# Kernel tuning notes

Hardware: AMD Instinct MI355X
Metric: run time of the kernel (lower is better)

Reference implementation:

```python
import jax, jax.numpy as jnp
import numpy as np

N = 100000   # total nodes in batched graph
E = 400000   # directed edges
F0 = 64      # Drug_Features
B = 512      # number of graphs
FINAL = 128  # Final_dim


def setup_inputs() -> dict:
    key = jax.random.key(0)
    ks = jax.random.split(key, 24)
    def w(k, shape, fan_in):
        return jax.random.normal(k, shape, dtype=jnp.float32) / np.sqrt(fan_in)
    inp = {
        "x": jax.random.normal(ks[0], (N, F0), dtype=jnp.float32),
        "edge_index": jax.random.randint(ks[1], (2, E), 0, N, dtype=jnp.int32),
        "batch": jnp.sort(jax.random.randint(ks[2], (N,), 0, B, dtype=jnp.int32)),
        "eps": jax.random.normal(ks[3], (N, 4 * F0), dtype=jnp.float32),
        # GCNConv weights: lin (in,out) no bias, separate bias added post-aggregation
        "W1": w(ks[4], (F0, 2 * F0), F0), "b1": jnp.zeros((2 * F0,), jnp.float32),
        "W2": w(ks[5], (2 * F0, 3 * F0), 2 * F0), "b2": jnp.zeros((3 * F0,), jnp.float32),
        "W3": w(ks[6], (3 * F0, 4 * F0), 3 * F0), "b3": jnp.zeros((4 * F0,), jnp.float32),
        "Wmu": w(ks[7], (4 * F0, 4 * F0), 4 * F0), "bmu": jnp.zeros((4 * F0,), jnp.float32),
        "Wlv": w(ks[8], (4 * F0, 4 * F0), 4 * F0), "blv": jnp.zeros((4 * F0,), jnp.float32),
        "fc1_w": w(ks[9], (4 * F0, 1024), 4 * F0), "fc1_b": jnp.zeros((1024,), jnp.float32),
        "fc2_w": w(ks[10], (1024, FINAL), 1024), "fc2_b": jnp.zeros((FINAL,), jnp.float32),
    }
    return inp


def reference(x, edge_index, batch, eps, W1, b1, W2, b2, W3, b3, Wmu, bmu, Wlv, blv,
              fc1_w, fc1_b, fc2_w, fc2_b):
    n = x.shape[0]
    row, col = edge_index[0], edge_index[1]
    loop = jnp.arange(n, dtype=row.dtype)
    row_f = jnp.concatenate([row, loop])  # with self-loops (PyG GCNConv default)
    col_f = jnp.concatenate([col, loop])
    deg = jax.ops.segment_sum(jnp.ones_like(col_f, dtype=x.dtype), col_f, num_segments=n)
    dinv = jnp.where(deg > 0, deg ** -0.5, 0.0)
    norm = (dinv[row_f] * dinv[col_f])[:, None]  # [E+N, 1]

    def gcn(h, W, b):
        m = h @ W                                   # transform first (out <= in here ok)
        agg = jax.ops.segment_sum(norm * m[row_f], col_f, num_segments=n)
        return agg + b

    h = jax.nn.relu(gcn(x, W1, b1))
    h = jax.nn.relu(gcn(h, W2, b2))
    h = jax.nn.relu(gcn(h, W3, b3))   # PMVO pre-pool features [N, 4F]
    mu = gcn(h, Wmu, bmu)
    logvar = gcn(h, Wlv, blv)
    std = jnp.exp(0.5 * logvar)
    amvo = mu + eps * std             # reparameterize
    x2 = jax.ops.segment_max(h, batch, num_segments=B)   # global max pool per graph
    pmvo = jax.nn.relu(x2 @ fc1_w + fc1_b) @ fc2_w + fc2_b  # dropout is identity (eval)
    return (amvo, mu, logvar, pmvo)
```

## Files before the change

### kernel.cpp

```cpp
#include <hip/hip_runtime.h>
#include <hip/hip_bf16.h>
#include <math.h>


#define THREADS 256

typedef short s8v __attribute__((ext_vector_type(8)));
typedef float f4v __attribute__((ext_vector_type(4)));

__device__ inline float bf_lo(unsigned int u) {
    union { unsigned int i; float f; } c; c.i = u << 16; return c.f;
}
__device__ inline float bf_hi(unsigned int u) {
    union { unsigned int i; float f; } c; c.i = u & 0xffff0000u; return c.f;
}
__device__ inline unsigned short f2bf(float f) {
    __hip_bfloat16 h = __float2bfloat16(f);
    return *reinterpret_cast<unsigned short*>(&h);
}
__device__ inline float bf2f(unsigned short u) {
    union { unsigned int i; float f; } c; c.i = ((unsigned int)u) << 16; return c.f;
}


__global__ void k_count(const int* __restrict__ col, int* __restrict__ counts, int E) {
    int e = blockIdx.x * blockDim.x + threadIdx.x;
    if (e < E) atomicAdd(&counts[col[e]], 1);
}

__global__ void k_dinv(const int* __restrict__ counts, float* __restrict__ dinv, int N) {
    int i = blockIdx.x * blockDim.x + threadIdx.x;
    if (i < N) dinv[i] = rsqrtf((float)(counts[i] + 1));
}

__global__ __launch_bounds__(1024) void k_scan(const int* __restrict__ counts,
                                               int* __restrict__ offsets, int N) {
    __shared__ int ssum[1024];
    int tid = threadIdx.x;
    int chunk = (N + 1023) / 1024;
    int begin = tid * chunk;
    int end = begin + chunk; if (end > N) end = N;
    int s = 0;
    for (int i = begin; i < end; ++i) s += counts[i] + 1;
    ssum[tid] = s;
    __syncthreads();
    for (int off = 1; off < 1024; off <<= 1) {
        int v = 0;
        if (tid >= off) v = ssum[tid - off];
        __syncthreads();
        if (tid >= off) ssum[tid] += v;
        __syncthreads();
    }
    int prefix = (tid == 0) ? 0 : ssum[tid - 1];
    for (int i = begin; i < end; ++i) {
        offsets[i] = prefix;
        prefix += counts[i] + 1;
    }
    if (end == N && begin < N) offsets[N] = prefix;
}

__global__ void k_init_cursor(const int* __restrict__ offsets, int* __restrict__ cursor, int N) {
    int i = blockIdx.x * blockDim.x + threadIdx.x;
    if (i < N) cursor[i] = offsets[i];
}

__global__ void k_scatter(const int* __restrict__ row, const int* __restrict__ col,
                          const float* __restrict__ dinv, int* __restrict__ cursor,
                          int* __restrict__ csr_row, float* __restrict__ csr_norm,
                          int E, int N) {
    int e = blockIdx.x * blockDim.x + threadIdx.x;
    if (e < E) {
        int r = row[e], c = col[e];
        int slot = atomicAdd(&cursor[c], 1);
        csr_row[slot] = r;
        csr_norm[slot] = dinv[r] * dinv[c];
    } else if (e < E + N) {
        int i = e - E;
        int slot = atomicAdd(&cursor[i], 1);
        csr_row[slot] = i;
        float d = dinv[i];
        csr_norm[slot] = d * d;
    }
}


__global__ void k_cast_bf16(const float* __restrict__ src, unsigned short* __restrict__ dst, int n) {
    int i = blockIdx.x * blockDim.x + threadIdx.x;
    if (i < n) dst[i] = f2bf(src[i]);
}

__global__ void k_prep_w(const float* __restrict__ W, unsigned short* __restrict__ WT,
                         int K, int Nc) {
    int id = blockIdx.x * blockDim.x + threadIdx.x;
    if (id < K * Nc) {
        int k = id / Nc, n = id % Nc;
        WT[(size_t)n * K + k] = f2bf(W[id]);
    }
}

__global__ void k_agg(const unsigned short* __restrict__ h,
                      const int* __restrict__ offsets,
                      const int* __restrict__ csr_row,
                      const float* __restrict__ csr_nrm,
                      unsigned short* __restrict__ g, int N, int F) {
    int node = blockIdx.x * blockDim.y + threadIdx.y;
    if (node >= N) return;
    int c8 = threadIdx.x * 8;
    int off0 = offsets[node], off1 = offsets[node + 1];
    float a0=0.f,a1=0.f,a2=0.f,a3=0.f,a4=0.f,a5=0.f,a6=0.f,a7=0.f;
    for (int sl = off0; sl < off1; ++sl) {
        int r = csr_row[sl];
        float w = csr_nrm[sl];
        uint4 v = *(const uint4*)(h + (size_t)r * F + c8);
        a0 += w * bf_lo(v.x); a1 += w * bf_hi(v.x);
        a2 += w * bf_lo(v.y); a3 += w * bf_hi(v.y);
        a4 += w * bf_lo(v.z); a5 += w * bf_hi(v.z);
        a6 += w * bf_lo(v.w); a7 += w * bf_hi(v.w);
    }
    uint4 o;
    o.x = (unsigned)f2bf(a0) | ((unsigned)f2bf(a1) << 16);
    o.y = (unsigned)f2bf(a2) | ((unsigned)f2bf(a3) << 16);
    o.z = (unsigned)f2bf(a4) | ((unsigned)f2bf(a5) << 16);
    o.w = (unsigned)f2bf(a6) | ((unsigned)f2bf(a7) << 16);
    *(uint4*)(g + (size_t)node * F + c8) = o;
}

#define GBM 128
#define GBN 64
#define GBK 64
#define LDP 72

__global__ __launch_bounds__(512) void k_gemm_mfma(
    const unsigned short* __restrict__ A,
    const unsigned short* __restrict__ WT,
    const float* __restrict__ bias,
    void* __restrict__ Cout, int M, int K, int Nc,
    int dorelu, int out_bf16) {
    __shared__ unsigned short sA[GBM * LDP];
    __shared__ unsigned short sB[GBN * LDP];
    const int tid = threadIdx.x;
    const int wave = tid >> 6;
    const int lane = tid & 63;
    const int bm = blockIdx.x * GBM;
    const int bn = blockIdx.y * GBN;

    f4v acc[4];
    #pragma unroll
    for (int j = 0; j < 4; ++j) acc[j] = (f4v){0.f, 0.f, 0.f, 0.f};

    const int lrow = tid >> 3;
    const int lk = (tid & 7) * 8;
    const int fr = lane & 15;
    const int fk = (lane >> 4) * 8;

    for (int k0 = 0; k0 < K; k0 += GBK) {
        #pragma unroll
        for (int p = 0; p < 2; ++p) {
            int r = lrow + p * 64;
            int gm = bm + r;
            uint4 v = make_uint4(0u, 0u, 0u, 0u);
            if (gm < M) v = *(const uint4*)(A + (size_t)gm * K + k0 + lk);
            *(uint4*)(&sA[r * LDP + lk]) = v;
        }
        {
            uint4 v = *(const uint4*)(WT + (size_t)(bn + lrow) * K + k0 + lk);
            *(uint4*)(&sB[lrow * LDP + lk]) = v;
        }
        __syncthreads();
        #pragma unroll
        for (int ks = 0; ks < 2; ++ks) {
            s8v a0 = *(const s8v*)(&sA[(wave * 16 + fr) * LDP + ks * 32 + fk]);
            #pragma unroll
            for (int nt = 0; nt < 4; ++nt) {
                s8v b = *(const s8v*)(&sB[(nt * 16 + fr) * LDP + ks * 32 + fk]);
                acc[nt] = __builtin_amdgcn_mfma_f32_16x16x32_bf16(a0, b, acc[nt], 0, 0, 0);
            }
        }
        __syncthreads();
    }

    const int col_l = lane & 15;
    const int row_q = (lane >> 4) * 4;
    #pragma unroll
    for (int nt = 0; nt < 4; ++nt) {
        #pragma unroll
        for (int i = 0; i < 4; ++i) {
            int row = bm + wave * 16 + row_q + i;
            int col = bn + nt * 16 + col_l;
            if (row < M) {
                float v = acc[nt][i] + bias[col];
                if (dorelu) v = fmaxf(v, 0.f);
                if (out_bf16)
                    ((unsigned short*)Cout)[(size_t)row * Nc + col] = f2bf(v);
                else
                    ((float*)Cout)[(size_t)row * Nc + col] = v;
            }
        }
    }
}

__global__ __launch_bounds__(512) void k_gemm_mfma_dual(
    const unsigned short* __restrict__ A,
    const unsigned short* __restrict__ WTm,
    const unsigned short* __restrict__ WTl,
    const float* __restrict__ bmu,
    const float* __restrict__ blv,
    const float* __restrict__ eps,
    float* __restrict__ mu,
    float* __restrict__ lv,
    float* __restrict__ amvo,
    int M, int K, int Nc) {
    __shared__ unsigned short sA[GBM * LDP];
    __shared__ unsigned short sBm[GBN * LDP];
    __shared__ unsigned short sBl[GBN * LDP];
    const int tid = threadIdx.x;
    const int wave = tid >> 6;
    const int lane = tid & 63;
    const int bm = blockIdx.x * GBM;
    const int bn = blockIdx.y * GBN;

    f4v accM[4], accL[4];
    #pragma unroll
    for (int j = 0; j < 4; ++j) {
        accM[j] = (f4v){0.f, 0.f, 0.f, 0.f};
        accL[j] = (f4v){0.f, 0.f, 0.f, 0.f};
    }

    const int lrow = tid >> 3;
    const int lk = (tid & 7) * 8;
    const int fr = lane & 15;
    const int fk = (lane >> 4) * 8;

    for (int k0 = 0; k0 < K; k0 += GBK) {
        #pragma unroll
        for (int p = 0; p < 2; ++p) {
            int r = lrow + p * 64;
            int gm = bm + r;
            uint4 v = make_uint4(0u, 0u, 0u, 0u);
            if (gm < M) v = *(const uint4*)(A + (size_t)gm * K + k0 + lk);
            *(uint4*)(&sA[r * LDP + lk]) = v;
        }
        {
            uint4 vm = *(const uint4*)(WTm + (size_t)(bn + lrow) * K + k0 + lk);
            uint4 vl = *(const uint4*)(WTl + (size_t)(bn + lrow) * K + k0 + lk);
            *(uint4*)(&sBm[lrow * LDP + lk]) = vm;
            *(uint4*)(&sBl[lrow * LDP + lk]) = vl;
        }
        __syncthreads();
        #pragma unroll
        for (int ks = 0; ks < 2; ++ks) {
            s8v a0 = *(const s8v*)(&sA[(wave * 16 + fr) * LDP + ks * 32 + fk]);
            #pragma unroll
            for (int nt = 0; nt < 4; ++nt) {
                s8v bm_ = *(const s8v*)(&sBm[(nt * 16 + fr) * LDP + ks * 32 + fk]);
                s8v bl_ = *(const s8v*)(&sBl[(nt * 16 + fr) * LDP + ks * 32 + fk]);
                accM[nt] = __builtin_amdgcn_mfma_f32_16x16x32_bf16(a0, bm_, accM[nt], 0, 0, 0);
                accL[nt] = __builtin_amdgcn_mfma_f32_16x16x32_bf16(a0, bl_, accL[nt], 0, 0, 0);
            }
        }
        __syncthreads();
    }

    const int col_l = lane & 15;
    const int row_q = (lane >> 4) * 4;
    #pragma unroll
    for (int nt = 0; nt < 4; ++nt) {
        int col = bn + nt * 16 + col_l;
        float bM = bmu[col];
        float bL = blv[col];
        #pragma unroll
        for (int i = 0; i < 4; ++i) {
            int row = bm + wave * 16 + row_q + i;
            if (row < M) {
                size_t idx = (size_t)row * Nc + col;
                float vm = accM[nt][i] + bM;
                float vl = accL[nt][i] + bL;
                mu[idx] = vm;
                lv[idx] = vl;
                amvo[idx] = vm + eps[idx] * expf(0.5f * vl);
            }
        }
    }
}

__global__ __launch_bounds__(256) void k_fc1(const float* __restrict__ x2,
                                             const float* __restrict__ W,
                                             const float* __restrict__ bias,
                                             float* __restrict__ hid,
                                             int K, int Nc) {
    const int m = blockIdx.x;
    const int t = threadIdx.x;
    __shared__ float sx[256];
    for (int k = t; k < K; k += 256) sx[k] = x2[(size_t)m * K + k];
    __syncthreads();
    const int nc4 = Nc >> 2;
    const float4* Wv = (const float4*)W;
    float4 acc = make_float4(0.f, 0.f, 0.f, 0.f);
    #pragma unroll 4
    for (int k = 0; k < K; ++k) {
        float a = sx[k];
        float4 w = Wv[(size_t)k * nc4 + t];
        acc.x += a * w.x; acc.y += a * w.y;
        acc.z += a * w.z; acc.w += a * w.w;
    }
    float4 b = ((const float4*)bias)[t];
    float4 r;
    r.x = fmaxf(acc.x + b.x, 0.f);
    r.y = fmaxf(acc.y + b.y, 0.f);
    r.z = fmaxf(acc.z + b.z, 0.f);
    r.w = fmaxf(acc.w + b.w, 0.f);
    ((float4*)hid)[(size_t)m * nc4 + t] = r;
}

__global__ __launch_bounds__(128) void k_fc2(const float* __restrict__ hid,
                                             const float* __restrict__ W,
                                             const float* __restrict__ bias,
                                             float* __restrict__ out,
                                             int K, int Nc) {
    const int m = blockIdx.x;
    const int c = threadIdx.x;
    __shared__ float sh[1024];
    for (int k = c; k < K; k += 128) sh[k] = hid[(size_t)m * K + k];
    __syncthreads();
    float a0 = 0.f, a1 = 0.f, a2 = 0.f, a3 = 0.f;
    for (int k = 0; k < K; k += 4) {
        a0 += sh[k    ] * W[(size_t)(k    ) * Nc + c];
        a1 += sh[k + 1] * W[(size_t)(k + 1) * Nc + c];
        a2 += sh[k + 2] * W[(size_t)(k + 2) * Nc + c];
        a3 += sh[k + 3] * W[(size_t)(k + 3) * Nc + c];
    }
    out[(size_t)m * Nc + c] = (a0 + a1) + (a2 + a3) + bias[c];
}


__global__ void k_gstart(const int* __restrict__ batch, int* __restrict__ gstart, int Nn, int B) {
    int b = blockIdx.x * blockDim.x + threadIdx.x;
    if (b > B) return;
    int lo = 0, hi = Nn;
    while (lo < hi) {
        int mid = (lo + hi) >> 1;
        if (batch[mid] < b) lo = mid + 1; else hi = mid;
    }
    gstart[b] = lo;
}

__global__ void k_pool_max(const unsigned short* __restrict__ h, const int* __restrict__ gstart,
                           float* __restrict__ x2, int F) {
    int b = blockIdx.x;
    int c = blockIdx.y * 64 + threadIdx.x;
    int s = gstart[b], e = gstart[b + 1];
    float mv = -INFINITY;
    for (int i = s + threadIdx.y; i < e; i += 4)
        mv = fmaxf(mv, bf2f(h[(size_t)i * F + c]));
    __shared__ float red[4][64];
    red[threadIdx.y][threadIdx.x] = mv;
    __syncthreads();
    if (threadIdx.y == 0) {
        mv = fmaxf(fmaxf(red[0][threadIdx.x], red[1][threadIdx.x]),
                   fmaxf(red[2][threadIdx.x], red[3][threadIdx.x]));
        x2[(size_t)b * F + c] = mv;
    }
}

static inline int ceil_div(int a, int b) { return (a + b - 1) / b; }

extern "C" void kernel_launch(void* const* d_in, const int* in_sizes, int n_in,
                              void* d_out, int out_size, void* d_ws, size_t ws_size,
                              hipStream_t stream) {
    const int F0 = 64;
    const int N = in_sizes[0] / F0;
    const int E = in_sizes[1] / 2;
    const int F4 = 4 * F0;
    const int B = (out_size - 3 * N * F4) / 128;
    const int M = E + N;

    const float* x     = (const float*)d_in[0];
    const int*   ei    = (const int*)d_in[1];
    const int*   batch = (const int*)d_in[2];
    const float* eps   = (const float*)d_in[3];
    const float* W1  = (const float*)d_in[4];  const float* b1  = (const float*)d_in[5];
    const float* W2  = (const float*)d_in[6];  const float* b2  = (const float*)d_in[7];
    const float* W3  = (const float*)d_in[8];  const float* b3  = (const float*)d_in[9];
    const float* Wmu = (const float*)d_in[10]; const float* bmu = (const float*)d_in[11];
    const float* Wlv = (const float*)d_in[12]; const float* blv = (const float*)d_in[13];
    const float* fc1w = (const float*)d_in[14]; const float* fc1b = (const float*)d_in[15];
    const float* fc2w = (const float*)d_in[16]; const float* fc2b = (const float*)d_in[17];

    const int* e_row = ei;
    const int* e_col = ei + E;

    float* out  = (float*)d_out;
    float* amvo = out;
    float* mu   = out + (size_t)N * F4;
    float* lv   = out + 2 * (size_t)N * F4;
    float* pmvo = out + 3 * (size_t)N * F4;

    char* w = (char*)d_ws;
    auto alloc = [&](size_t bytes) -> void* {
        void* p = (void*)w;
        w += (bytes + 255) & ~(size_t)255;
        return p;
    };
    float* dinv    = (float*)alloc((size_t)N * 4);
    int*   counts  = (int*)alloc((size_t)N * 4);
    int*   offsets = (int*)alloc((size_t)(N + 1) * 4);
    int*   csr_row = (int*)alloc((size_t)M * 4);
    float* csr_nrm = (float*)alloc((size_t)M * 4);
    int*   gstart  = (int*)alloc((size_t)(B + 1) * 4);
    unsigned short* xb  = (unsigned short*)alloc((size_t)N * F0 * 2);
    unsigned short* h1  = (unsigned short*)alloc((size_t)N * 128 * 2);
    unsigned short* h2  = (unsigned short*)alloc((size_t)N * 192 * 2);
    unsigned short* h3  = (unsigned short*)alloc((size_t)N * 256 * 2);
    unsigned short* g   = (unsigned short*)alloc((size_t)N * 256 * 2);
    unsigned short* wt1 = (unsigned short*)alloc((size_t)64 * 128 * 2);
    unsigned short* wt2 = (unsigned short*)alloc((size_t)128 * 192 * 2);
    unsigned short* wt3 = (unsigned short*)alloc((size_t)192 * 256 * 2);
    unsigned short* wtm = (unsigned short*)alloc((size_t)256 * 256 * 2);
    unsigned short* wtl = (unsigned short*)alloc((size_t)256 * 256 * 2);
    float* x2  = (float*)alloc((size_t)B * F4 * 4);
    float* hid = (float*)alloc((size_t)B * 1024 * 4);
    (void)ws_size; (void)n_in;

    hipMemsetAsync(counts, 0, (size_t)N * 4, stream);
    k_count<<<ceil_div(E, THREADS), THREADS, 0, stream>>>(e_col, counts, E);
    k_dinv<<<ceil_div(N, THREADS), THREADS, 0, stream>>>(counts, dinv, N);
    k_scan<<<1, 1024, 0, stream>>>(counts, offsets, N);
    k_init_cursor<<<ceil_div(N, THREADS), THREADS, 0, stream>>>(offsets, counts, N);
    k_scatter<<<ceil_div(E + N, THREADS), THREADS, 0, stream>>>(
        e_row, e_col, dinv, counts, csr_row, csr_nrm, E, N);

    k_cast_bf16<<<ceil_div(N * F0, THREADS), THREADS, 0, stream>>>(x, xb, N * F0);
    k_prep_w<<<ceil_div(64 * 128, THREADS), THREADS, 0, stream>>>(W1, wt1, 64, 128);
    k_prep_w<<<ceil_div(128 * 192, THREADS), THREADS, 0, stream>>>(W2, wt2, 128, 192);
    k_prep_w<<<ceil_div(192 * 256, THREADS), THREADS, 0, stream>>>(W3, wt3, 192, 256);
    k_prep_w<<<ceil_div(256 * 256, THREADS), THREADS, 0, stream>>>(Wmu, wtm, 256, 256);
    k_prep_w<<<ceil_div(256 * 256, THREADS), THREADS, 0, stream>>>(Wlv, wtl, 256, 256);

    {
        dim3 blk(8, 32);
        k_agg<<<ceil_div(N, 32), blk, 0, stream>>>(xb, offsets, csr_row, csr_nrm, g, N, 64);
        dim3 gg(ceil_div(N, GBM), 128 / GBN);
        k_gemm_mfma<<<gg, 512, 0, stream>>>(g, wt1, b1, h1, N, 64, 128, 1, 1);
    }
    {
        dim3 blk(16, 16);
        k_agg<<<ceil_div(N, 16), blk, 0, stream>>>(h1, offsets, csr_row, csr_nrm, g, N, 128);
        dim3 gg(ceil_div(N, GBM), 192 / GBN);
        k_gemm_mfma<<<gg, 512, 0, stream>>>(g, wt2, b2, h2, N, 128, 192, 1, 1);
    }
    {
        dim3 blk(24, 8);
        k_agg<<<ceil_div(N, 8), blk, 0, stream>>>(h2, offsets, csr_row, csr_nrm, g, N, 192);
        dim3 gg(ceil_div(N, GBM), 256 / GBN);
        k_gemm_mfma<<<gg, 512, 0, stream>>>(g, wt3, b3, h3, N, 192, 256, 1, 1);
    }
    {
        dim3 blk(32, 8);
        k_agg<<<ceil_div(N, 8), blk, 0, stream>>>(h3, offsets, csr_row, csr_nrm, g, N, 256);
        dim3 gg(ceil_div(N, GBM), 256 / GBN);
        k_gemm_mfma_dual<<<gg, 512, 0, stream>>>(g, wtm, wtl, bmu, blv, eps,
                                                 mu, lv, amvo, N, 256, 256);
    }

    k_gstart<<<ceil_div(B + 1, THREADS), THREADS, 0, stream>>>(batch, gstart, N, B);
    {
        dim3 gg(B, F4 / 64);
        dim3 blk(64, 4);
        k_pool_max<<<gg, blk, 0, stream>>>(h3, gstart, x2, F4);
    }
    k_fc1<<<B, 256, 0, stream>>>(x2, fc1w, fc1b, hid, F4, 1024);
    k_fc2<<<B, 128, 0, stream>>>(hid, fc2w, fc2b, pmvo, 1024, 128);
}
```

Baseline: 1.108 ms.

## Stage full-K weight tile in LDS, read A directly, group block order for L2 reuse

The MFMA GEMM kernels now load the block's whole weight slice (all K) into shared memory once and read A fragments straight from global memory into registers. This removes the per-K-step A staging through LDS and the two barriers per iteration. Blocks are launched on a 1D grid and remapped so that eight M-tiles sweep all N-tiles together, which is meant to improve L2 reuse of A across column tiles. The trade-off is larger LDS use (the dual kernel holds two 64x264 tiles, lowering occupancy) and uncoalesced, non-shared A loads where each wave fetches its own rows per K step.

```diff
diff --git a/kernel.cpp b/kernel.cpp
--- a/kernel.cpp
+++ b/kernel.cpp
@@ -128,7 +128,7 @@
 #define GBM 128
 #define GBN 64
 #define GBK 64
-#define LDP 72
+#define LDBMAX 264
 
 __global__ __launch_bounds__(512) void k_gemm_mfma(
     const unsigned short* __restrict__ A,
@@ -136,47 +136,52 @@
     const float* __restrict__ bias,
     void* __restrict__ Cout, int M, int K, int Nc,
     int dorelu, int out_bf16) {
-    __shared__ unsigned short sA[GBM * LDP];
-    __shared__ unsigned short sB[GBN * LDP];
+    __shared__ unsigned short sB[64 * LDBMAX];
     const int tid = threadIdx.x;
     const int wave = tid >> 6;
     const int lane = tid & 63;
-    const int bm = blockIdx.x * GBM;
-    const int bn = blockIdx.y * GBN;
+
+    const int nbm = (M + GBM - 1) / GBM;
+    const int NB = Nc >> 6;
+    const int grpsz = 8 * NB;
+    const int id = blockIdx.x;
+    const int bmi = (id / grpsz) * 8 + (id % 8);
+    const int bni = (id % grpsz) >> 3;
+    if (bmi >= nbm) return;
+    const int bm = bmi * GBM;
+    const int bn = bni * GBN;
+
+    const int ldb = K + 8;
+    const int kc8 = K >> 3;
+    for (int l = tid; l < 64 * kc8; l += 512) {
+        int row = l / kc8, kc = (l - row * kc8) * 8;
+        *(uint4*)(&sB[row * ldb + kc]) =
+            *(const uint4*)(WT + (size_t)(bn + row) * K + kc);
+    }
+    __syncthreads();
 
     f4v acc[4];
     #pragma unroll
     for (int j = 0; j < 4; ++j) acc[j] = (f4v){0.f, 0.f, 0.f, 0.f};
 
-    const int lrow = tid >> 3;
-    const int lk = (tid & 7) * 8;
     const int fr = lane & 15;
     const int fk = (lane >> 4) * 8;
+    const int gm = bm + wave * 16 + fr;
+    const unsigned short* Arow = A + (size_t)gm * K;
+    const bool inM = (gm < M);
 
     for (int k0 = 0; k0 < K; k0 += GBK) {
         #pragma unroll
-        for (int p = 0; p < 2; ++p) {
-            int r = lrow + p * 64;
-            int gm = bm + r;
-            uint4 v = make_uint4(0u, 0u, 0u, 0u);
-            if (gm < M) v = *(const uint4*)(A + (size_t)gm * K + k0 + lk);
-            *(uint4*)(&sA[r * LDP + lk]) = v;
-        }
-        {
-            uint4 v = *(const uint4*)(WT + (size_t)(bn + lrow) * K + k0 + lk);
-            *(uint4*)(&sB[lrow * LDP + lk]) = v;
-        }
-        __syncthreads();
-        #pragma unroll
         for (int ks = 0; ks < 2; ++ks) {
-            s8v a0 = *(const s8v*)(&sA[(wave * 16 + fr) * LDP + ks * 32 + fk]);
+            int kk = k0 + ks * 32 + fk;
+            s8v a0 = inM ? *(const s8v*)(Arow + kk)
+                         : (s8v){0, 0, 0, 0, 0, 0, 0, 0};
             #pragma unroll
             for (int nt = 0; nt < 4; ++nt) {
-                s8v b = *(const s8v*)(&sB[(nt * 16 + fr) * LDP + ks * 32 + fk]);
+                s8v b = *(const s8v*)(&sB[(nt * 16 + fr) * ldb + kk]);
                 acc[nt] = __builtin_amdgcn_mfma_f32_16x16x32_bf16(a0, b, acc[nt], 0, 0, 0);
             }
         }
-        __syncthreads();
     }
 
     const int col_l = lane & 15;
@@ -210,14 +215,32 @@
     float* __restrict__ lv,
     float* __restrict__ amvo,
     int M, int K, int Nc) {
-    __shared__ unsigned short sA[GBM * LDP];
-    __shared__ unsigned short sBm[GBN * LDP];
-    __shared__ unsigned short sBl[GBN * LDP];
+    __shared__ unsigned short sBm[64 * LDBMAX];
+    __shared__ unsigned short sBl[64 * LDBMAX];
     const int tid = threadIdx.x;
     const int wave = tid >> 6;
     const int lane = tid & 63;
-    const int bm = blockIdx.x * GBM;
-    const int bn = blockIdx.y * GBN;
+
+    const int nbm = (M + GBM - 1) / GBM;
+    const int NB = Nc >> 6;
+    const int grpsz = 8 * NB;
+    const int id = blockIdx.x;
+    const int bmi = (id / grpsz) * 8 + (id % 8);
+    const int bni = (id % grpsz) >> 3;
+    if (bmi >= nbm) return;
+    const int bm = bmi * GBM;
+    const int bn = bni * GBN;
+
+    const int ldb = K + 8;
+    const int kc8 = K >> 3;
+    for (int l = tid; l < 64 * kc8; l += 512) {
+        int row = l / kc8, kc = (l - row * kc8) * 8;
+        *(uint4*)(&sBm[row * ldb + kc]) =
+            *(const uint4*)(WTm + (size_t)(bn + row) * K + kc);
+        *(uint4*)(&sBl[row * ldb + kc]) =
+            *(const uint4*)(WTl + (size_t)(bn + row) * K + kc);
+    }
+    __syncthreads();
 
     f4v accM[4], accL[4];
     #pragma unroll
@@ -226,39 +249,26 @@
         accL[j] = (f4v){0.f, 0.f, 0.f, 0.f};
     }
 
-    const int lrow = tid >> 3;
-    const int lk = (tid & 7) * 8;
     const int fr = lane & 15;
     const int fk = (lane >> 4) * 8;
+    const int gm = bm + wave * 16 + fr;
+    const unsigned short* Arow = A + (size_t)gm * K;
+    const bool inM = (gm < M);
 
     for (int k0 = 0; k0 < K; k0 += GBK) {
         #pragma unroll
-        for (int p = 0; p < 2; ++p) {
-            int r = lrow + p * 64;
-            int gm = bm + r;
-            uint4 v = make_uint4(0u, 0u, 0u, 0u);
-            if (gm < M) v = *(const uint4*)(A + (size_t)gm * K + k0 + lk);
-            *(uint4*)(&sA[r * LDP + lk]) = v;
-        }
-        {
-            uint4 vm = *(const uint4*)(WTm + (size_t)(bn + lrow) * K + k0 + lk);
-            uint4 vl = *(const uint4*)(WTl + (size_t)(bn + lrow) * K + k0 + lk);
-            *(uint4*)(&sBm[lrow * LDP + lk]) = vm;
-            *(uint4*)(&sBl[lrow * LDP + lk]) = vl;
-        }
-        __syncthreads();
-        #pragma unroll
         for (int ks = 0; ks < 2; ++ks) {
-            s8v a0 = *(const s8v*)(&sA[(wave * 16 + fr) * LDP + ks * 32 + fk]);
+            int kk = k0 + ks * 32 + fk;
+            s8v a0 = inM ? *(const s8v*)(Arow + kk)
+                         : (s8v){0, 0, 0, 0, 0, 0, 0, 0};
             #pragma unroll
             for (int nt = 0; nt < 4; ++nt) {
-                s8v bm_ = *(const s8v*)(&sBm[(nt * 16 + fr) * LDP + ks * 32 + fk]);
-                s8v bl_ = *(const s8v*)(&sBl[(nt * 16 + fr) * LDP + ks * 32 + fk]);
+                s8v bm_ = *(const s8v*)(&sBm[(nt * 16 + fr) * ldb + kk]);
+                s8v bl_ = *(const s8v*)(&sBl[(nt * 16 + fr) * ldb + kk]);
                 accM[nt] = __builtin_amdgcn_mfma_f32_16x16x32_bf16(a0, bm_, accM[nt], 0, 0, 0);
                 accL[nt] = __builtin_amdgcn_mfma_f32_16x16x32_bf16(a0, bl_, accL[nt], 0, 0, 0);
             }
         }
-        __syncthreads();
     }
 
     const int col_l = lane & 15;
@@ -436,30 +446,29 @@
     k_prep_w<<<ceil_div(256 * 256, THREADS), THREADS, 0, stream>>>(Wmu, wtm, 256, 256);
     k_prep_w<<<ceil_div(256 * 256, THREADS), THREADS, 0, stream>>>(Wlv, wtl, 256, 256);
 
+    const int nbm = ceil_div(N, GBM);
+    const int nbm8 = ceil_div(nbm, 8) * 8;
+
     {
         dim3 blk(8, 32);
         k_agg<<<ceil_div(N, 32), blk, 0, stream>>>(xb, offsets, csr_row, csr_nrm, g, N, 64);
-        dim3 gg(ceil_div(N, GBM), 128 / GBN);
-        k_gemm_mfma<<<gg, 512, 0, stream>>>(g, wt1, b1, h1, N, 64, 128, 1, 1);
+        k_gemm_mfma<<<nbm8 * 2, 512, 0, stream>>>(g, wt1, b1, h1, N, 64, 128, 1, 1);
     }
     {
         dim3 blk(16, 16);
         k_agg<<<ceil_div(N, 16), blk, 0, stream>>>(h1, offsets, csr_row, csr_nrm, g, N, 128);
-        dim3 gg(ceil_div(N, GBM), 192 / GBN);
-        k_gemm_mfma<<<gg, 512, 0, stream>>>(g, wt2, b2, h2, N, 128, 192, 1, 1);
+        k_gemm_mfma<<<nbm8 * 3, 512, 0, stream>>>(g, wt2, b2, h2, N, 128, 192, 1, 1);
     }
     {
         dim3 blk(24, 8);
         k_agg<<<ceil_div(N, 8), blk, 0, stream>>>(h2, offsets, csr_row, csr_nrm, g, N, 192);
-        dim3 gg(ceil_div(N, GBM), 256 / GBN);
-        k_gemm_mfma<<<gg, 512, 0, stream>>>(g, wt3, b3, h3, N, 192, 256, 1, 1);
+        k_gemm_mfma<<<nbm8 * 4, 512, 0, stream>>>(g, wt3, b3, h3, N, 192, 256, 1, 1);
     }
     {
         dim3 blk(32, 8);
         k_agg<<<ceil_div(N, 8), blk, 0, stream>>>(h3, offsets, csr_row, csr_nrm, g, N, 256);
-        dim3 gg(ceil_div(N, GBM), 256 / GBN);
-        k_gemm_mfma_dual<<<gg, 512, 0, stream>>>(g, wtm, wtl, bmu, blv, eps,
-                                                 mu, lv, amvo, N, 256, 256);
+        k_gemm_mfma_dual<<<nbm8 * 4, 512, 0, stream>>>(g, wtm, wtl, bmu, blv, eps,
+                                                       mu, lv, amvo, N, 256, 256);
     }
 
     k_gstart<<<ceil_div(B + 1, THREADS), THREADS, 0, stream>>>(batch, gstart, N, B);
```

Measured after the change: 1.096 ms. About the same (-1.0%).

## Fuse GCN neighbor aggregation into MFMA GEMM via shared-memory tile

Applied to the files above, without the earlier changes.

Each layer's CSR aggregation is merged into the following MFMA GEMM. A block aggregates 128 nodes into a shared-memory bf16 tile, then loops over all output column groups, reading transposed weights directly from global memory instead of staging them in LDS. This drops the intermediate g buffer round-trip and four kernel launches. In exchange, the grid shrinks to about 782 blocks with large LDS use, which lowers occupancy. The aggregation gather and the GEMM phase can no longer overlap across blocks the way separate kernels allowed, and weight fragments now come from global memory and cache.

```diff
diff --git a/kernel.cpp b/kernel.cpp
--- a/kernel.cpp
+++ b/kernel.cpp
@@ -98,109 +98,89 @@
     }
 }
 
-__global__ void k_agg(const unsigned short* __restrict__ h,
-                      const int* __restrict__ offsets,
-                      const int* __restrict__ csr_row,
-                      const float* __restrict__ csr_nrm,
-                      unsigned short* __restrict__ g, int N, int F) {
-    int node = blockIdx.x * blockDim.y + threadIdx.y;
-    if (node >= N) return;
-    int c8 = threadIdx.x * 8;
-    int off0 = offsets[node], off1 = offsets[node + 1];
-    float a0=0.f,a1=0.f,a2=0.f,a3=0.f,a4=0.f,a5=0.f,a6=0.f,a7=0.f;
-    for (int sl = off0; sl < off1; ++sl) {
-        int r = csr_row[sl];
-        float w = csr_nrm[sl];
-        uint4 v = *(const uint4*)(h + (size_t)r * F + c8);
-        a0 += w * bf_lo(v.x); a1 += w * bf_hi(v.x);
-        a2 += w * bf_lo(v.y); a3 += w * bf_hi(v.y);
-        a4 += w * bf_lo(v.z); a5 += w * bf_hi(v.z);
-        a6 += w * bf_lo(v.w); a7 += w * bf_hi(v.w);
-    }
-    uint4 o;
-    o.x = (unsigned)f2bf(a0) | ((unsigned)f2bf(a1) << 16);
-    o.y = (unsigned)f2bf(a2) | ((unsigned)f2bf(a3) << 16);
-    o.z = (unsigned)f2bf(a4) | ((unsigned)f2bf(a5) << 16);
-    o.w = (unsigned)f2bf(a6) | ((unsigned)f2bf(a7) << 16);
-    *(uint4*)(g + (size_t)node * F + c8) = o;
-}
-
-#define GBM 128
-#define GBN 64
-#define GBK 64
-#define LDP 72
-
-__global__ __launch_bounds__(512) void k_gemm_mfma(
-    const unsigned short* __restrict__ A,
+template<int K, int NCG>
+__global__ __launch_bounds__(512) void k_fused_relu(
+    const unsigned short* __restrict__ h,
+    const int* __restrict__ offsets,
+    const int* __restrict__ csr_row,
+    const float* __restrict__ csr_nrm,
     const unsigned short* __restrict__ WT,
     const float* __restrict__ bias,
-    void* __restrict__ Cout, int M, int K, int Nc,
-    int dorelu, int out_bf16) {
-    __shared__ unsigned short sA[GBM * LDP];
-    __shared__ unsigned short sB[GBN * LDP];
+    unsigned short* __restrict__ out,
+    int N) {
+    constexpr int LDB = K + 8;
+    constexpr int CH = K / 8;
+    constexpr int Nc = NCG * 64;
+    __shared__ unsigned short sG[128 * LDB];
     const int tid = threadIdx.x;
+    const int bm = blockIdx.x * 128;
+
+    for (int task = tid; task < 128 * CH; task += 512) {
+        const int ln = task / CH;
+        const int c8 = (task - ln * CH) * 8;
+        const int node = bm + ln;
+        uint4 o = make_uint4(0u, 0u, 0u, 0u);
+        if (node < N) {
+            float a0=0.f,a1=0.f,a2=0.f,a3=0.f,a4=0.f,a5=0.f,a6=0.f,a7=0.f;
+            const int off0 = offsets[node], off1 = offsets[node + 1];
+            for (int sl = off0; sl < off1; ++sl) {
+                int r = csr_row[sl];
+                float w = csr_nrm[sl];
+                uint4 v = *(const uint4*)(h + (size_t)r * K + c8);
+                a0 += w * bf_lo(v.x); a1 += w * bf_hi(v.x);
+                a2 += w * bf_lo(v.y); a3 += w * bf_hi(v.y);
+                a4 += w * bf_lo(v.z); a5 += w * bf_hi(v.z);
+                a6 += w * bf_lo(v.w); a7 += w * bf_hi(v.w);
+            }
+            o.x = (unsigned)f2bf(a0) | ((unsigned)f2bf(a1) << 16);
+            o.y = (unsigned)f2bf(a2) | ((unsigned)f2bf(a3) << 16);
+            o.z = (unsigned)f2bf(a4) | ((unsigned)f2bf(a5) << 16);
+            o.w = (unsigned)f2bf(a6) | ((unsigned)f2bf(a7) << 16);
+        }
+        *(uint4*)(&sG[ln * LDB + c8]) = o;
+    }
+    __syncthreads();
+
     const int wave = tid >> 6;
     const int lane = tid & 63;
-    const int bm = blockIdx.x * GBM;
-    const int bn = blockIdx.y * GBN;
-
-    f4v acc[4];
-    #pragma unroll
-    for (int j = 0; j < 4; ++j) acc[j] = (f4v){0.f, 0.f, 0.f, 0.f};
-
-    const int lrow = tid >> 3;
-    const int lk = (tid & 7) * 8;
     const int fr = lane & 15;
     const int fk = (lane >> 4) * 8;
-
-    for (int k0 = 0; k0 < K; k0 += GBK) {
-        #pragma unroll
-        for (int p = 0; p < 2; ++p) {
-            int r = lrow + p * 64;
-            int gm = bm + r;
-            uint4 v = make_uint4(0u, 0u, 0u, 0u);
-            if (gm < M) v = *(const uint4*)(A + (size_t)gm * K + k0 + lk);
-            *(uint4*)(&sA[r * LDP + lk]) = v;
-        }
-        {
-            uint4 v = *(const uint4*)(WT + (size_t)(bn + lrow) * K + k0 + lk);
-            *(uint4*)(&sB[lrow * LDP + lk]) = v;
-        }
-        __syncthreads();
-        #pragma unroll
-        for (int ks = 0; ks < 2; ++ks) {
-            s8v a0 = *(const s8v*)(&sA[(wave * 16 + fr) * LDP + ks * 32 + fk]);
+    const int col_l = lane & 15;
+    const int row_q = (lane >> 4) * 4;
+
+    for (int cg = 0; cg < NCG; ++cg) {
+        f4v acc[4];
+        #pragma unroll
+        for (int j = 0; j < 4; ++j) acc[j] = (f4v){0.f, 0.f, 0.f, 0.f};
+        #pragma unroll
+        for (int k0 = 0; k0 < K; k0 += 32) {
+            const int kk = k0 + fk;
+            s8v a0 = *(const s8v*)(&sG[(wave * 16 + fr) * LDB + kk]);
             #pragma unroll
             for (int nt = 0; nt < 4; ++nt) {
-                s8v b = *(const s8v*)(&sB[(nt * 16 + fr) * LDP + ks * 32 + fk]);
+                s8v b = *(const s8v*)(WT + (size_t)(cg * 64 + nt * 16 + fr) * K + kk);
                 acc[nt] = __builtin_amdgcn_mfma_f32_16x16x32_bf16(a0, b, acc[nt], 0, 0, 0);
             }
         }
-        __syncthreads();
-    }
-
-    const int col_l = lane & 15;
-    const int row_q = (lane >> 4) * 4;
-    #pragma unroll
-    for (int nt = 0; nt < 4; ++nt) {
-        #pragma unroll
-        for (int i = 0; i < 4; ++i) {
-            int row = bm + wave * 16 + row_q + i;
-            int col = bn + nt * 16 + col_l;
-            if (row < M) {
-                float v = acc[nt][i] + bias[col];
-                if (dorelu) v = fmaxf(v, 0.f);
-                if (out_bf16)
-                    ((unsigned short*)Cout)[(size_t)row * Nc + col] = f2bf(v);
-                else
-                    ((float*)Cout)[(size_t)row * Nc + col] = v;
-            }
-        }
-    }
-}
-
-__global__ __launch_bounds__(512) void k_gemm_mfma_dual(
-    const unsigned short* __restrict__ A,
+        #pragma unroll
+        for (int nt = 0; nt < 4; ++nt) {
+            const int col = cg * 64 + nt * 16 + col_l;
+            const float bb = bias[col];
+            #pragma unroll
+            for (int i = 0; i < 4; ++i) {
+                int row = bm + wave * 16 + row_q + i;
+                if (row < N)
+                    out[(size_t)row * Nc + col] = f2bf(fmaxf(acc[nt][i] + bb, 0.f));
+            }
+        }
+    }
+}
+
+__global__ __launch_bounds__(512) void k_fused_dual(
+    const unsigned short* __restrict__ h,
+    const int* __restrict__ offsets,
+    const int* __restrict__ csr_row,
+    const float* __restrict__ csr_nrm,
     const unsigned short* __restrict__ WTm,
     const unsigned short* __restrict__ WTl,
     const float* __restrict__ bmu,
@@ -209,75 +189,84 @@
     float* __restrict__ mu,
     float* __restrict__ lv,
     float* __restrict__ amvo,
-    int M, int K, int Nc) {
-    __shared__ unsigned short sA[GBM * LDP];
-    __shared__ unsigned short sBm[GBN * LDP];
-    __shared__ unsigned short sBl[GBN * LDP];
+    int N) {
+    constexpr int K = 256;
+    constexpr int LDB = K + 8;
+    constexpr int CH = K / 8;
+    constexpr int Nc = 256;
+    __shared__ unsigned short sG[128 * LDB];
     const int tid = threadIdx.x;
+    const int bm = blockIdx.x * 128;
+
+    for (int task = tid; task < 128 * CH; task += 512) {
+        const int ln = task / CH;
+        const int c8 = (task - ln * CH) * 8;
+        const int node = bm + ln;
+        uint4 o = make_uint4(0u, 0u, 0u, 0u);
+        if (node < N) {
+            float a0=0.f,a1=0.f,a2=0.f,a3=0.f,a4=0.f,a5=0.f,a6=0.f,a7=0.f;
+            const int off0 = offsets[node], off1 = offsets[node + 1];
+            for (int sl = off0; sl < off1; ++sl) {
+                int r = csr_row[sl];
+                float w = csr_nrm[sl];
+                uint4 v = *(const uint4*)(h + (size_t)r * K + c8);
+                a0 += w * bf_lo(v.x); a1 += w * bf_hi(v.x);
+                a2 += w * bf_lo(v.y); a3 += w * bf_hi(v.y);
+                a4 += w * bf_lo(v.z); a5 += w * bf_hi(v.z);
+                a6 += w * bf_lo(v.w); a7 += w * bf_hi(v.w);
+            }
+            o.x = (unsigned)f2bf(a0) | ((unsigned)f2bf(a1) << 16);
+            o.y = (unsigned)f2bf(a2) | ((unsigned)f2bf(a3) << 16);
+            o.z = (unsigned)f2bf(a4) | ((unsigned)f2bf(a5) << 16);
+            o.w = (unsigned)f2bf(a6) | ((unsigned)f2bf(a7) << 16);
+        }
+        *(uint4*)(&sG[ln * LDB + c8]) = o;
+    }
+    __syncthreads();
+
     const int wave = tid >> 6;
     const int lane = tid & 63;
-    const int bm = blockIdx.x * GBM;
-    const int bn = blockIdx.y * GBN;
-
-    f4v accM[4], accL[4];
-    #pragma unroll
-    for (int j = 0; j < 4; ++j) {
-        accM[j] = (f4v){0.f, 0.f, 0.f, 0.f};
-        accL[j] = (f4v){0.f, 0.f, 0.f, 0.f};
-    }
-
-    const int lrow = tid >> 3;
-    const int lk = (tid & 7) * 8;
     const int fr = lane & 15;
     const int fk = (lane >> 4) * 8;
-
-    for (int k0 = 0; k0 < K; k0 += GBK) {
-        #pragma unroll
-        for (int p = 0; p < 2; ++p) {
-            int r = lrow + p * 64;
-            int gm = bm + r;
-            uint4 v = make_uint4(0u, 0u, 0u, 0u);
-            if (gm < M) v = *(const uint4*)(A + (size_t)gm * K + k0 + lk);
-            *(uint4*)(&sA[r * LDP + lk]) = v;
-        }
-        {
-            uint4 vm = *(const uint4*)(WTm + (size_t)(bn + lrow) * K + k0 + lk);
-            uint4 vl = *(const uint4*)(WTl + (size_t)(bn + lrow) * K + k0 + lk);
-            *(uint4*)(&sBm[lrow * LDP + lk]) = vm;
-            *(uint4*)(&sBl[lrow * LDP + lk]) = vl;
-        }
-        __syncthreads();
-        #pragma unroll
-        for (int ks = 0; ks < 2; ++ks) {
-            s8v a0 = *(const s8v*)(&sA[(wave * 16 + fr) * LDP + ks * 32 + fk]);
+    const int col_l = lane & 15;
+    const int row_q = (lane >> 4) * 4;
+
+    for (int cg = 0; cg < 4; ++cg) {
+        f4v accM[4], accL[4];
+        #pragma unroll
+        for (int j = 0; j < 4; ++j) {
+            accM[j] = (f4v){0.f, 0.f, 0.f, 0.f};
+            accL[j] = (f4v){0.f, 0.f, 0.f, 0.f};
+        }
+        #pragma unroll
+        for (int k0 = 0; k0 < K; k0 += 32) {
+            const int kk = k0 + fk;
+            s8v a0 = *(const s8v*)(&sG[(wave * 16 + fr) * LDB + kk]);
             #pragma unroll
             for (int nt = 0; nt < 4; ++nt) {
-                s8v bm_ = *(const s8v*)(&sBm[(nt * 16 + fr) * LDP + ks * 32 + fk]);
-                s8v bl_ = *(const s8v*)(&sBl[(nt * 16 + fr) * LDP + ks * 32 + fk]);
+                const size_t woff = (size_t)(cg * 64 + nt * 16 + fr) * K + kk;
+                s8v bm_ = *(const s8v*)(WTm + woff);
+                s8v bl_ = *(const s8v*)(WTl + woff);
                 accM[nt] = __builtin_amdgcn_mfma_f32_16x16x32_bf16(a0, bm_, accM[nt], 0, 0, 0);
                 accL[nt] = __builtin_amdgcn_mfma_f32_16x16x32_bf16(a0, bl_, accL[nt], 0, 0, 0);
             }
         }
-        __syncthreads();
-    }
-
-    const int col_l = lane & 15;
-    const int row_q = (lane >> 4) * 4;
-    #pragma unroll
-    for (int nt = 0; nt < 4; ++nt) {
-        int col = bn + nt * 16 + col_l;
-        float bM = bmu[col];
-        float bL = blv[col];
-        #pragma unroll
-        for (int i = 0; i < 4; ++i) {
-            int row = bm + wave * 16 + row_q + i;
-            if (row < M) {
-                size_t idx = (size_t)row * Nc + col;
-                float vm = accM[nt][i] + bM;
-                float vl = accL[nt][i] + bL;
-                mu[idx] = vm;
-                lv[idx] = vl;
-                amvo[idx] = vm + eps[idx] * expf(0.5f * vl);
+        #pragma unroll
+        for (int nt = 0; nt < 4; ++nt) {
+            const int col = cg * 64 + nt * 16 + col_l;
+            const float bM = bmu[col];
+            const float bL = blv[col];
+            #pragma unroll
+            for (int i = 0; i < 4; ++i) {
+                int row = bm + wave * 16 + row_q + i;
+                if (row < N) {
+                    size_t idx = (size_t)row * Nc + col;
+                    float vm = accM[nt][i] + bM;
+                    float vl = accL[nt][i] + bL;
+                    mu[idx] = vm;
+                    lv[idx] = vl;
+                    amvo[idx] = vm + eps[idx] * expf(0.5f * vl);
+                }
             }
         }
     }
@@ -411,7 +400,6 @@
     unsigned short* h1  = (unsigned short*)alloc((size_t)N * 128 * 2);
     unsigned short* h2  = (unsigned short*)alloc((size_t)N * 192 * 2);
     unsigned short* h3  = (unsigned short*)alloc((size_t)N * 256 * 2);
-    unsigned short* g   = (unsigned short*)alloc((size_t)N * 256 * 2);
     unsigned short* wt1 = (unsigned short*)alloc((size_t)64 * 128 * 2);
     unsigned short* wt2 = (unsigned short*)alloc((size_t)128 * 192 * 2);
     unsigned short* wt3 = (unsigned short*)alloc((size_t)192 * 256 * 2);
@@ -436,31 +424,17 @@
     k_prep_w<<<ceil_div(256 * 256, THREADS), THREADS, 0, stream>>>(Wmu, wtm, 256, 256);
     k_prep_w<<<ceil_div(256 * 256, THREADS), THREADS, 0, stream>>>(Wlv, wtl, 256, 256);
 
-    {
-        dim3 blk(8, 32);
-        k_agg<<<ceil_div(N, 32), blk, 0, stream>>>(xb, offsets, csr_row, csr_nrm, g, N, 64);
-        dim3 gg(ceil_div(N, GBM), 128 / GBN);
-        k_gemm_mfma<<<gg, 512, 0, stream>>>(g, wt1, b1, h1, N, 64, 128, 1, 1);
-    }
-    {
-        dim3 blk(16, 16);
-        k_agg<<<ceil_div(N, 16), blk, 0, stream>>>(h1, offsets, csr_row, csr_nrm, g, N, 128);
-        dim3 gg(ceil_div(N, GBM), 192 / GBN);
-        k_gemm_mfma<<<gg, 512, 0, stream>>>(g, wt2, b2, h2, N, 128, 192, 1, 1);
-    }
-    {
-        dim3 blk(24, 8);
-        k_agg<<<ceil_div(N, 8), blk, 0, stream>>>(h2, offsets, csr_row, csr_nrm, g, N, 192);
-        dim3 gg(ceil_div(N, GBM), 256 / GBN);
-        k_gemm_mfma<<<gg, 512, 0, stream>>>(g, wt3, b3, h3, N, 192, 256, 1, 1);
-    }
-    {
-        dim3 blk(32, 8);
-        k_agg<<<ceil_div(N, 8), blk, 0, stream>>>(h3, offsets, csr_row, csr_nrm, g, N, 256);
-        dim3 gg(ceil_div(N, GBM), 256 / GBN);
-        k_gemm_mfma_dual<<<gg, 512, 0, stream>>>(g, wtm, wtl, bmu, blv, eps,
-                                                 mu, lv, amvo, N, 256, 256);
-    }
+    const int nbm = ceil_div(N, 128);
+
+    k_fused_relu<64, 2><<<nbm, 512, 0, stream>>>(
+        xb, offsets, csr_row, csr_nrm, wt1, b1, h1, N);
+    k_fused_relu<128, 3><<<nbm, 512, 0, stream>>>(
+        h1, offsets, csr_row, csr_nrm, wt2, b2, h2, N);
+    k_fused_relu<192, 4><<<nbm, 512, 0, stream>>>(
+        h2, offsets, csr_row, csr_nrm, wt3, b3, h3, N);
+    k_fused_dual<<<nbm, 512, 0, stream>>>(
+        h3, offsets, csr_row, csr_nrm, wtm, wtl, bmu, blv, eps,
+        mu, lv, amvo, N);
 
     k_gstart<<<ceil_div(B + 1, THREADS), THREADS, 0, stream>>>(batch, gstart, N, B);
     {
```

Measured after the change: 1.475 ms. 33.1% more time.
